# Performance work log

Hardware: AMD Instinct MI355X
Metric: run time of the kernel (lower is better)

The kernel has to match this reference:

```python
import jax, jax.numpy as jnp
import numpy as np

KH, KW = 3, 3          # kernel_size
SH, SW = 1, 1          # strides
EM_ITERS = 3           # standard EM routing iteration count
EPS = 1e-9


def to_blocks(x):
    """im2col-style block extraction matching ConvCaps2D._to_blocks.
    x: [B, H, W, ...] -> [B, Ho, Wo, KH, KW, ...] with Ho=(H-KH+1)//SH."""
    Ho = (x.shape[1] - KH + 1) // SH
    Wo = (x.shape[2] - KW + 1) // SW
    rows = []
    for i in range(KH):
        cols = [x[:, i:i + (Ho - 1) * SH + 1:SH, j:j + (Wo - 1) * SW + 1:SW]
                for j in range(KW)]
        rows.append(jnp.stack(cols, axis=3))   # [B,Ho,Wo,KW,...]
    return jnp.stack(rows, axis=3)             # [B,Ho,Wo,KH,KW,...]


def em_routing(votes, a_in, beta_a, beta_u):
    """EM routing (Hinton et al. 2018 matrix capsules).
    votes: [B,Ho,Wo,O,N,D], a_in: [B,Ho,Wo,N], beta_*: [1,1,1,O].
    Returns poses mu [B,Ho,Wo,O,D], activations [B,Ho,Wo,O]."""
    B, Ho, Wo, O, N, D = votes.shape
    R = jnp.full((B, Ho, Wo, O, N), 1.0 / O, dtype=votes.dtype)
    a = a_in[:, :, :, None, :]                                  # [B,Ho,Wo,1,N]
    mu = None
    a_out = None
    for t in range(EM_ITERS):
        inv_temp = 1.0 + t                                      # increasing lambda schedule
        # ---- M-step ----
        r = R * a                                               # [B,Ho,Wo,O,N]
        r_sum = jnp.sum(r, axis=-1, keepdims=True) + EPS        # [B,Ho,Wo,O,1]
        mu = jnp.einsum('bhwon,bhwond->bhwod', r, votes) / r_sum
        diff2 = (votes - mu[:, :, :, :, None, :]) ** 2          # [B,Ho,Wo,O,N,D]
        sigma2 = jnp.einsum('bhwon,bhwond->bhwod', r, diff2) / r_sum + EPS
        cost = jnp.sum((beta_u[..., None] + 0.5 * jnp.log(sigma2)) * r_sum, axis=-1)
        a_out = jax.nn.sigmoid(inv_temp * (beta_a - cost))      # [B,Ho,Wo,O]
        # ---- E-step (skipped after last M-step) ----
        if t < EM_ITERS - 1:
            s2 = sigma2[:, :, :, :, None, :]
            logp = -0.5 * jnp.sum(jnp.log(2.0 * jnp.pi * s2) + diff2 / s2, axis=-1)
            logits = jnp.log(a_out + EPS)[..., None] + logp     # [B,Ho,Wo,O,N]
            R = jax.nn.softmax(logits, axis=3)                  # normalize over output caps
    return mu, a_out


def setup_inputs() -> dict:
    key = jax.random.key(0)
    k1, k2, k3, k4, k5 = jax.random.split(key, 5)
    B, H, W, Cin, d1, d2 = 4, 16, 16, 16, 4, 4
    O = 32
    poses = jax.random.normal(k1, (B, H, W, Cin, d1, d2), dtype=jnp.float32)
    activations = jax.random.uniform(k2, (B, H, W, Cin), dtype=jnp.float32)
    fan_in = KH * KW * Cin * d1 * d2
    kernel = jax.random.normal(k3, (O, KH, KW, Cin, d1, d2), dtype=jnp.float32) * np.sqrt(2.0 / fan_in).astype(np.float32)
    beta_a = jax.random.normal(k4, (1, 1, 1, O), dtype=jnp.float32) * 0.1
    beta_u = jax.random.normal(k5, (1, 1, 1, O), dtype=jnp.float32) * 0.1
    return {"poses": poses, "activations": activations, "kernel": kernel,
            "beta_a": beta_a, "beta_u": beta_u}


def reference(poses, activations, kernel, beta_a, beta_u):
    B, _, _, Cin, d1, d2 = poses.shape
    O = kernel.shape[0]
    pose_blocks = to_blocks(poses)                              # [B,Ho,Wo,KH,KW,Cin,d1,d2]
    # votes = pose @ W per (output channel, kernel offset, input channel)
    votes = jnp.einsum('bhwKLcij,oKLcjl->bhwoKLcil', pose_blocks, kernel)
    Ho, Wo = votes.shape[1], votes.shape[2]
    N = KH * KW * Cin
    votes = votes.reshape(B, Ho, Wo, O, N, d1 * d2)             # [B,Ho,Wo,O,N,D]
    a_blocks = to_blocks(activations).reshape(B, Ho, Wo, N)
    mu, a_out = em_routing(votes, a_blocks, beta_a, beta_u)
    capsule_poses = mu.reshape(B, Ho, Wo, O, d1, d2)
    return capsule_poses, a_out
```

## Files before the change

kernel.cpp:

```cpp
#include <hip/hip_runtime.h>
#include <math.h>

#define NBLK 784
#define O_ 32
#define N_ 144
#define D_ 16
#define PS 20
#define RS 148

__global__ __launch_bounds__(256) void convcaps_em(
    const float* __restrict__ poses,
    const float* __restrict__ acts,
    const float* __restrict__ kern,
    const float* __restrict__ beta_a,
    const float* __restrict__ beta_u,
    float* __restrict__ out)
{
    const int pix = blockIdx.x;
    const int b  = pix / 196;
    const int hw = pix - b * 196;
    const int ho = hw / 14;
    const int wo = hw - ho * 14;

    __shared__ __align__(16) float P[N_ * PS];
    __shared__ float A[N_];
    __shared__ float Rm[O_ * RS];

    const int t = threadIdx.x;

    for (int idx = t; idx < N_ * D_; idx += 256) {
        int n = idx >> 4, d = idx & 15;
        int ki = n / 48, kj = (n >> 4) - ki * 3, c = n & 15;
        P[n * PS + d] = poses[((b * 16 + ho + ki) * 16 + (wo + kj)) * 256 + c * 16 + d];
    }
    if (t < N_) {
        int n = t;
        int ki = n / 48, kj = (n >> 4) - ki * 3, c = n & 15;
        A[n] = acts[((b * 16 + ho + ki) * 16 + (wo + kj)) * 16 + c];
    }
    __syncthreads();
    for (int idx = t; idx < O_ * N_; idx += 256) {
        int oo = idx / N_;
        int nn = idx - oo * N_;
        Rm[oo * RS + nn] = 0.03125f * A[nn];
    }
    __syncthreads();

    const int o = t >> 3;
    const int s = t & 7;
    const float buv = beta_u[o];
    const float ba  = beta_a[o];
    const float* Kbase = kern + (size_t)o * (N_ * D_);

    float a_out = 0.f;
    float mu[16];

    for (int it = 0; it < 3; ++it) {
        float S1[16], S2[16];
#pragma unroll
        for (int d = 0; d < 16; ++d) { S1[d] = 0.f; S2[d] = 0.f; }
        float rs = 0.f;

#pragma unroll 2
        for (int k = 0; k < 18; ++k) {
            const int n = s + (k << 3);
            const float r = Rm[o * RS + n];
            rs += r;
            float pv[16], kv[16];
            const float4* Pp = (const float4*)(P + n * PS);
            ((float4*)pv)[0] = Pp[0];
            ((float4*)pv)[1] = Pp[1];
            ((float4*)pv)[2] = Pp[2];
            ((float4*)pv)[3] = Pp[3];
            const float4* Kp = (const float4*)(Kbase + n * D_);
            ((float4*)kv)[0] = Kp[0];
            ((float4*)kv)[1] = Kp[1];
            ((float4*)kv)[2] = Kp[2];
            ((float4*)kv)[3] = Kp[3];
#pragma unroll
            for (int i = 0; i < 4; ++i) {
#pragma unroll
                for (int l = 0; l < 4; ++l) {
                    float v = fmaf(pv[i*4+0], kv[0+l],
                              fmaf(pv[i*4+1], kv[4+l],
                              fmaf(pv[i*4+2], kv[8+l],
                                   pv[i*4+3] * kv[12+l])));
                    S1[i*4+l] = fmaf(r, v, S1[i*4+l]);
                    S2[i*4+l] = fmaf(r * v, v, S2[i*4+l]);
                }
            }
        }

#pragma unroll
        for (int m = 1; m < 8; m <<= 1) {
            rs += __shfl_xor(rs, m, 64);
#pragma unroll
            for (int d = 0; d < 16; ++d) {
                S1[d] += __shfl_xor(S1[d], m, 64);
                S2[d] += __shfl_xor(S2[d], m, 64);
            }
        }

        rs += 1e-9f;
        const float inv_rs = 1.0f / rs;
        float sig[16];
#pragma unroll
        for (int d = 0; d < 16; ++d) {
            mu[d] = S1[d] * inv_rs;
            sig[d] = fmaf(-mu[d], mu[d], S2[d] * inv_rs) + 1e-9f;
        }
        const float L = __logf(sig[0]  * sig[1])  + __logf(sig[2]  * sig[3])
                      + __logf(sig[4]  * sig[5])  + __logf(sig[6]  * sig[7])
                      + __logf(sig[8]  * sig[9])  + __logf(sig[10] * sig[11])
                      + __logf(sig[12] * sig[13]) + __logf(sig[14] * sig[15]);
        const float cost = rs * fmaf(0.5f, L, 16.0f * buv);
        const float x = (float)(it + 1) * (ba - cost);
        a_out = 1.0f / (1.0f + __expf(-x));

        if (it < 2) {
            float isg[16];
#pragma unroll
            for (int d = 0; d < 16; ++d) isg[d] = 1.0f / sig[d];
            const float LC = __logf(a_out + 1e-9f)
                           - 0.5f * (16.0f * 1.8378770664093453f + L);
            __syncthreads();

#pragma unroll 2
            for (int k = 0; k < 18; ++k) {
                const int n = s + (k << 3);
                float pv[16], kv[16];
                const float4* Pp = (const float4*)(P + n * PS);
                ((float4*)pv)[0] = Pp[0];
                ((float4*)pv)[1] = Pp[1];
                ((float4*)pv)[2] = Pp[2];
                ((float4*)pv)[3] = Pp[3];
                const float4* Kp = (const float4*)(Kbase + n * D_);
                ((float4*)kv)[0] = Kp[0];
                ((float4*)kv)[1] = Kp[1];
                ((float4*)kv)[2] = Kp[2];
                ((float4*)kv)[3] = Kp[3];
                float Q = 0.f;
#pragma unroll
                for (int i = 0; i < 4; ++i) {
#pragma unroll
                    for (int l = 0; l < 4; ++l) {
                        float v = fmaf(pv[i*4+0], kv[0+l],
                                  fmaf(pv[i*4+1], kv[4+l],
                                  fmaf(pv[i*4+2], kv[8+l],
                                       pv[i*4+3] * kv[12+l])));
                        const float df = v - mu[i*4+l];
                        Q = fmaf(df * df, isg[i*4+l], Q);
                    }
                }
                Rm[o * RS + n] = fmaf(-0.5f, Q, LC);
            }
            __syncthreads();

            if (t < N_) {
                float v[32];
                float mx = -1e30f;
#pragma unroll
                for (int oo = 0; oo < 32; ++oo) {
                    v[oo] = Rm[oo * RS + t];
                    mx = fmaxf(mx, v[oo]);
                }
                float sm = 0.f;
#pragma unroll
                for (int oo = 0; oo < 32; ++oo) {
                    v[oo] = __expf(v[oo] - mx);
                    sm += v[oo];
                }
                const float sc = A[t] / sm;
#pragma unroll
                for (int oo = 0; oo < 32; ++oo)
                    Rm[oo * RS + t] = v[oo] * sc;
            }
            __syncthreads();
        }
    }

    if (s == 0) {
        float4* ob = (float4*)(out + (size_t)pix * 512 + o * 16);
        ob[0] = make_float4(mu[0],  mu[1],  mu[2],  mu[3]);
        ob[1] = make_float4(mu[4],  mu[5],  mu[6],  mu[7]);
        ob[2] = make_float4(mu[8],  mu[9],  mu[10], mu[11]);
        ob[3] = make_float4(mu[12], mu[13], mu[14], mu[15]);
        out[401408 + pix * 32 + o] = a_out;
    }
}

extern "C" void kernel_launch(void* const* d_in, const int* in_sizes, int n_in,
                              void* d_out, int out_size, void* d_ws, size_t ws_size,
                              hipStream_t stream)
{
    const float* poses  = (const float*)d_in[0];
    const float* acts   = (const float*)d_in[1];
    const float* kern   = (const float*)d_in[2];
    const float* beta_a = (const float*)d_in[3];
    const float* beta_u = (const float*)d_in[4];
    float* out = (float*)d_out;
    convcaps_em<<<NBLK, 256, 0, stream>>>(poses, acts, kern, beta_a, beta_u, out);
}
```

Measured before the change: 102.5 us.

## Split EM routing into per-iteration M-step and E-step kernels over workspace

Replaces the single fused kernel (one block per output pixel, 784 blocks) with five launches that alternate an M-step kernel (grid 784x4, 128 threads) and an E-step/softmax kernel (grid 784x6). Routing weights and per-capsule statistics are passed through the workspace buffer. The goal is more parallelism and occupancy than 784 large blocks with heavy shared memory can give. In exchange it adds launch overhead, global-memory round trips for R and stats, and recomputation of votes from global poses in every kernel. The old fused kernel remains as a fallback when the workspace is too small.

```diff
diff --git a/kernel.cpp b/kernel.cpp
--- a/kernel.cpp
+++ b/kernel.cpp
@@ -7,6 +7,229 @@
 #define D_ 16
 #define PS 20
 #define RS 148
+
+#define STATS_STRIDE 36
+#define WS_STATS_FLOATS (25088 * STATS_STRIDE)
+#define WS_R_FLOATS     (784 * 32 * 144)
+#define WS_NEED_BYTES   ((size_t)(WS_STATS_FLOATS + WS_R_FLOATS) * 4)
+
+
+__global__ __launch_bounds__(128) void caps_mom(
+    const float* __restrict__ poses,
+    const float* __restrict__ acts,
+    const float* __restrict__ kern,
+    const float* __restrict__ Rw,
+    const float* __restrict__ beta_a,
+    const float* __restrict__ beta_u,
+    float* __restrict__ stats,
+    float* __restrict__ out,
+    int rmode, int fin, float invtemp)
+{
+    const int pix = blockIdx.x;
+    const int b  = pix / 196;
+    const int hw = pix - b * 196;
+    const int ho = hw / 14;
+    const int wo = hw - ho * 14;
+
+    const int t  = threadIdx.x;
+    const int o  = blockIdx.y * 8 + (t >> 4);
+    const int s  = t & 15;
+
+    const float* Kbase = kern + (size_t)o * (N_ * D_);
+    const float* Rrow  = Rw + ((size_t)pix * 32 + o) * 144;
+
+    float S1[16], S2[16];
+#pragma unroll
+    for (int d = 0; d < 16; ++d) { S1[d] = 0.f; S2[d] = 0.f; }
+    float rs = 0.f;
+
+#pragma unroll
+    for (int k = 0; k < 9; ++k) {
+        const int n = s + (k << 4);
+        const int ki = n / 48, kj = (n >> 4) - (n / 48) * 3, c = n & 15;
+        const int cell = (b * 16 + ho + ki) * 16 + (wo + kj);
+        float r;
+        if (rmode) r = Rrow[n];
+        else       r = acts[cell * 16 + c] * 0.03125f;
+        rs += r;
+        float pv[16], kv[16];
+        const float4* Pp = (const float4*)(poses + (size_t)cell * 256 + c * 16);
+        ((float4*)pv)[0] = Pp[0];
+        ((float4*)pv)[1] = Pp[1];
+        ((float4*)pv)[2] = Pp[2];
+        ((float4*)pv)[3] = Pp[3];
+        const float4* Kp = (const float4*)(Kbase + n * D_);
+        ((float4*)kv)[0] = Kp[0];
+        ((float4*)kv)[1] = Kp[1];
+        ((float4*)kv)[2] = Kp[2];
+        ((float4*)kv)[3] = Kp[3];
+#pragma unroll
+        for (int i = 0; i < 4; ++i) {
+#pragma unroll
+            for (int l = 0; l < 4; ++l) {
+                float v = fmaf(pv[i*4+0], kv[0+l],
+                          fmaf(pv[i*4+1], kv[4+l],
+                          fmaf(pv[i*4+2], kv[8+l],
+                               pv[i*4+3] * kv[12+l])));
+                S1[i*4+l] = fmaf(r, v, S1[i*4+l]);
+                S2[i*4+l] = fmaf(r * v, v, S2[i*4+l]);
+            }
+        }
+    }
+
+#pragma unroll
+    for (int m = 1; m < 16; m <<= 1) {
+        rs += __shfl_xor(rs, m, 64);
+#pragma unroll
+        for (int d = 0; d < 16; ++d) {
+            S1[d] += __shfl_xor(S1[d], m, 64);
+            S2[d] += __shfl_xor(S2[d], m, 64);
+        }
+    }
+
+    rs += 1e-9f;
+    const float inv_rs = 1.0f / rs;
+    float mu[16], sig[16];
+#pragma unroll
+    for (int d = 0; d < 16; ++d) {
+        mu[d] = S1[d] * inv_rs;
+        sig[d] = fmaf(-mu[d], mu[d], S2[d] * inv_rs) + 1e-9f;
+    }
+    const float L = __logf(sig[0]  * sig[1])  + __logf(sig[2]  * sig[3])
+                  + __logf(sig[4]  * sig[5])  + __logf(sig[6]  * sig[7])
+                  + __logf(sig[8]  * sig[9])  + __logf(sig[10] * sig[11])
+                  + __logf(sig[12] * sig[13]) + __logf(sig[14] * sig[15]);
+    const float cost = rs * fmaf(0.5f, L, 16.0f * beta_u[o]);
+    const float x = invtemp * (beta_a[o] - cost);
+    const float a_out = 1.0f / (1.0f + __expf(-x));
+
+    if (s == 0) {
+        if (fin) {
+            float4* ob = (float4*)(out + (size_t)pix * 512 + o * 16);
+            ob[0] = make_float4(mu[0],  mu[1],  mu[2],  mu[3]);
+            ob[1] = make_float4(mu[4],  mu[5],  mu[6],  mu[7]);
+            ob[2] = make_float4(mu[8],  mu[9],  mu[10], mu[11]);
+            ob[3] = make_float4(mu[12], mu[13], mu[14], mu[15]);
+            out[401408 + pix * 32 + o] = a_out;
+        } else {
+            float* sb = stats + ((size_t)pix * 32 + o) * STATS_STRIDE;
+            float4* sb4 = (float4*)sb;
+            sb4[0] = make_float4(mu[0],  mu[1],  mu[2],  mu[3]);
+            sb4[1] = make_float4(mu[4],  mu[5],  mu[6],  mu[7]);
+            sb4[2] = make_float4(mu[8],  mu[9],  mu[10], mu[11]);
+            sb4[3] = make_float4(mu[12], mu[13], mu[14], mu[15]);
+            float isg[16];
+#pragma unroll
+            for (int d = 0; d < 16; ++d) isg[d] = 1.0f / sig[d];
+            sb4[4] = make_float4(isg[0],  isg[1],  isg[2],  isg[3]);
+            sb4[5] = make_float4(isg[4],  isg[5],  isg[6],  isg[7]);
+            sb4[6] = make_float4(isg[8],  isg[9],  isg[10], isg[11]);
+            sb4[7] = make_float4(isg[12], isg[13], isg[14], isg[15]);
+            sb[32] = __logf(a_out + 1e-9f)
+                   - 0.5f * (16.0f * 1.8378770664093453f + L);
+        }
+    }
+}
+
+__global__ __launch_bounds__(256) void caps_logits(
+    const float* __restrict__ poses,
+    const float* __restrict__ acts,
+    const float* __restrict__ kern,
+    const float* __restrict__ stats,
+    float* __restrict__ Rw)
+{
+    const int pix  = blockIdx.x;
+    const int slab = blockIdx.y;
+    const int b  = pix / 196;
+    const int hw = pix - b * 196;
+    const int ho = hw / 14;
+    const int wo = hw - ho * 14;
+
+    const int t  = threadIdx.x;
+    const int o  = t >> 3;
+    const int ln = t & 7;
+
+    __shared__ float Lg[24][33];
+    __shared__ float Al[24];
+    __shared__ float Rl[32][24];
+
+    if (t < 24) {
+        const int n = slab * 24 + t;
+        const int ki = n / 48, kj = (n >> 4) - (n / 48) * 3, c = n & 15;
+        Al[t] = acts[((b * 16 + ho + ki) * 16 + (wo + kj)) * 16 + c];
+    }
+
+    float mu[16], isg[16];
+    const float* sb = stats + ((size_t)pix * 32 + o) * STATS_STRIDE;
+    const float4* sb4 = (const float4*)sb;
+    ((float4*)mu)[0]  = sb4[0]; ((float4*)mu)[1]  = sb4[1];
+    ((float4*)mu)[2]  = sb4[2]; ((float4*)mu)[3]  = sb4[3];
+    ((float4*)isg)[0] = sb4[4]; ((float4*)isg)[1] = sb4[5];
+    ((float4*)isg)[2] = sb4[6]; ((float4*)isg)[3] = sb4[7];
+    const float LC = sb[32];
+
+    const float* Kbase = kern + (size_t)o * (N_ * D_);
+
+#pragma unroll
+    for (int j = 0; j < 3; ++j) {
+        const int nl = ln * 3 + j;
+        const int n  = slab * 24 + nl;
+        const int ki = n / 48, kj = (n >> 4) - (n / 48) * 3, c = n & 15;
+        const int cell = (b * 16 + ho + ki) * 16 + (wo + kj);
+        float pv[16], kv[16];
+        const float4* Pp = (const float4*)(poses + (size_t)cell * 256 + c * 16);
+        ((float4*)pv)[0] = Pp[0];
+        ((float4*)pv)[1] = Pp[1];
+        ((float4*)pv)[2] = Pp[2];
+        ((float4*)pv)[3] = Pp[3];
+        const float4* Kp = (const float4*)(Kbase + n * D_);
+        ((float4*)kv)[0] = Kp[0];
+        ((float4*)kv)[1] = Kp[1];
+        ((float4*)kv)[2] = Kp[2];
+        ((float4*)kv)[3] = Kp[3];
+        float Q = 0.f;
+#pragma unroll
+        for (int i = 0; i < 4; ++i) {
+#pragma unroll
+            for (int l = 0; l < 4; ++l) {
+                float v = fmaf(pv[i*4+0], kv[0+l],
+                          fmaf(pv[i*4+1], kv[4+l],
+                          fmaf(pv[i*4+2], kv[8+l],
+                               pv[i*4+3] * kv[12+l])));
+                const float df = v - mu[i*4+l];
+                Q = fmaf(df * df, isg[i*4+l], Q);
+            }
+        }
+        Lg[nl][o] = fmaf(-0.5f, Q, LC);
+    }
+    __syncthreads();
+
+    if (t < 24) {
+        float mx = -1e30f;
+#pragma unroll
+        for (int oo = 0; oo < 32; ++oo) mx = fmaxf(mx, Lg[t][oo]);
+        float sm = 0.f;
+        float ev[32];
+#pragma unroll
+        for (int oo = 0; oo < 32; ++oo) {
+            ev[oo] = __expf(Lg[t][oo] - mx);
+            sm += ev[oo];
+        }
+        const float sc = Al[t] / sm;
+#pragma unroll
+        for (int oo = 0; oo < 32; ++oo) Rl[oo][t] = ev[oo] * sc;
+    }
+    __syncthreads();
+
+#pragma unroll
+    for (int rep = 0; rep < 3; ++rep) {
+        const int idx = t + rep * 256;
+        const int oo = idx / 24;
+        const int nl = idx - oo * 24;
+        Rw[((size_t)pix * 32 + oo) * 144 + slab * 24 + nl] = Rl[oo][nl];
+    }
+}
+
 
 __global__ __launch_bounds__(256) void convcaps_em(
     const float* __restrict__ poses,
@@ -199,5 +422,20 @@
     const float* beta_a = (const float*)d_in[3];
     const float* beta_u = (const float*)d_in[4];
     float* out = (float*)d_out;
-    convcaps_em<<<NBLK, 256, 0, stream>>>(poses, acts, kern, beta_a, beta_u, out);
+
+    if (ws_size >= WS_NEED_BYTES) {
+        float* stats = (float*)d_ws;
+        float* Rw    = stats + WS_STATS_FLOATS;
+        dim3 gm(NBLK, 4), gl(NBLK, 6);
+        caps_mom<<<gm, 128, 0, stream>>>(poses, acts, kern, Rw, beta_a, beta_u,
+                                         stats, out, 0, 0, 1.0f);
+        caps_logits<<<gl, 256, 0, stream>>>(poses, acts, kern, stats, Rw);
+        caps_mom<<<gm, 128, 0, stream>>>(poses, acts, kern, Rw, beta_a, beta_u,
+                                         stats, out, 1, 0, 2.0f);
+        caps_logits<<<gl, 256, 0, stream>>>(poses, acts, kern, stats, Rw);
+        caps_mom<<<gm, 128, 0, stream>>>(poses, acts, kern, Rw, beta_a, beta_u,
+                                         stats, out, 1, 1, 3.0f);
+    } else {
+        convcaps_em<<<NBLK, 256, 0, stream>>>(poses, acts, kern, beta_a, beta_u, out);
+    }
 }
```

Result: slower. 211.0 us (+105.9%).

## Fuse E-step softmax into M-step via lane-per-output layout with DPP reductions

Applied to the files above, without the earlier changes.

Remaps threads so the 32 output capsules sit in adjacent lanes and 8 groups split the inputs. The softmax over outputs is then done in registers with DPP/swizzle cross-lane max and sum, which removes the separate E-step vote pass, the shared R matrix, and several barriers. Each vote is computed once per iteration instead of twice. The partial sums are reduced across groups through a large shared buffer (about 33 KB), which adds LDS traffic and may lower occupancy. It also expands the quadratic form so the per-vote E-step needs fewer operations.

```diff
diff --git a/kernel.cpp b/kernel.cpp
--- a/kernel.cpp
+++ b/kernel.cpp
@@ -2,11 +2,104 @@
 #include <math.h>
 
 #define NBLK 784
-#define O_ 32
-#define N_ 144
-#define D_ 16
 #define PS 20
-#define RS 148
+#define LOG2PI_16 29.406033062549525f
+
+#define REDN (33 * 256)
+
+#define DPPF(x, ctrl) __int_as_float(__builtin_amdgcn_update_dpp(              \
+    0, __float_as_int(x), ctrl, 0xF, 0xF, true))
+
+__device__ __forceinline__ float swzx16(float x) {
+    return __int_as_float(__builtin_amdgcn_ds_swizzle(__float_as_int(x), 0x401F));
+}
+__device__ __forceinline__ float rmax32(float x) {
+    x = fmaxf(x, DPPF(x, 0xB1));
+    x = fmaxf(x, DPPF(x, 0x4E));
+    x = fmaxf(x, DPPF(x, 0x141));
+    x = fmaxf(x, DPPF(x, 0x140));
+    x = fmaxf(x, swzx16(x));
+    return x;
+}
+__device__ __forceinline__ float rsum32(float x) {
+    x += DPPF(x, 0xB1);
+    x += DPPF(x, 0x4E);
+    x += DPPF(x, 0x141);
+    x += DPPF(x, 0x140);
+    x += swzx16(x);
+    return x;
+}
+
+#define VOTE(kk, v) do {                                                       \
+        float pv[16], kv[16];                                                  \
+        const float4* Pp_ = (const float4*)(Pbase + (kk) * (8 * PS));          \
+        ((float4*)pv)[0] = Pp_[0]; ((float4*)pv)[1] = Pp_[1];                  \
+        ((float4*)pv)[2] = Pp_[2]; ((float4*)pv)[3] = Pp_[3];                  \
+        const float4* Kp_ = (const float4*)(Kg + (kk) * (8 * 16));             \
+        ((float4*)kv)[0] = Kp_[0]; ((float4*)kv)[1] = Kp_[1];                  \
+        ((float4*)kv)[2] = Kp_[2]; ((float4*)kv)[3] = Kp_[3];                  \
+        _Pragma("unroll")                                                      \
+        for (int i_ = 0; i_ < 4; ++i_) {                                       \
+            _Pragma("unroll")                                                  \
+            for (int l_ = 0; l_ < 4; ++l_) {                                   \
+                v[i_*4+l_] = fmaf(pv[i_*4+0], kv[0+l_],                        \
+                             fmaf(pv[i_*4+1], kv[4+l_],                        \
+                             fmaf(pv[i_*4+2], kv[8+l_],                        \
+                                  pv[i_*4+3] * kv[12+l_])));                   \
+            }                                                                  \
+        }                                                                      \
+    } while (0)
+
+#define REDUCE_G() do {                                                        \
+    __syncthreads();                                                           \
+    _Pragma("unroll")                                                          \
+    for (int j = 0; j < 16; ++j) {                                             \
+        Red[j * 256 + t]        = S1[j];                                       \
+        Red[(j + 16) * 256 + t] = S2[j];                                       \
+    }                                                                          \
+    Red[32 * 256 + t] = rs;                                                    \
+    __syncthreads();                                                           \
+    _Pragma("unroll")                                                          \
+    for (int j = 0; j < 16; ++j) { S1[j] = 0.f; S2[j] = 0.f; }                 \
+    rs = 0.f;                                                                  \
+    _Pragma("unroll")                                                          \
+    for (int gg = 0; gg < 8; ++gg) {                                           \
+        const int base_ = gg * 32 + o;                                         \
+        _Pragma("unroll")                                                      \
+        for (int j = 0; j < 16; ++j) {                                         \
+            S1[j] += Red[j * 256 + base_];                                     \
+            S2[j] += Red[(j + 16) * 256 + base_];                              \
+        }                                                                      \
+        rs += Red[32 * 256 + base_];                                           \
+    }                                                                          \
+} while (0)
+
+#define STATS(IT) do {                                                         \
+    rs += 1e-9f;                                                               \
+    const float ivr_ = 1.0f / rs;                                              \
+    _Pragma("unroll")                                                          \
+    for (int j = 0; j < 16; ++j) {                                             \
+        mu[j]  = S1[j] * ivr_;                                                 \
+        sig[j] = fmaf(-mu[j], mu[j], S2[j] * ivr_) + 1e-9f;                    \
+    }                                                                          \
+    L = __logf(sig[0]  * sig[1])  + __logf(sig[2]  * sig[3])                   \
+      + __logf(sig[4]  * sig[5])  + __logf(sig[6]  * sig[7])                   \
+      + __logf(sig[8]  * sig[9])  + __logf(sig[10] * sig[11])                  \
+      + __logf(sig[12] * sig[13]) + __logf(sig[14] * sig[15]);                 \
+    const float cost_ = rs * fmaf(0.5f, L, 16.0f * buv);                       \
+    a_out = 1.0f / (1.0f + __expf(-(IT) * (ba - cost_)));                      \
+} while (0)
+
+#define PREP() do {                                                            \
+    float c0_ = 0.f;                                                           \
+    _Pragma("unroll")                                                          \
+    for (int j = 0; j < 16; ++j) {                                             \
+        isg[j] = 1.0f / sig[j];                                                \
+        qb[j]  = -2.0f * mu[j] * isg[j];                                       \
+        c0_    = fmaf(mu[j] * mu[j], isg[j], c0_);                             \
+    }                                                                          \
+    LC = __logf(a_out + 1e-9f) - 0.5f * (LOG2PI_16 + L) - 0.5f * c0_;          \
+} while (0)
 
 __global__ __launch_bounds__(256) void convcaps_em(
     const float* __restrict__ poses,
@@ -22,164 +115,88 @@
     const int ho = hw / 14;
     const int wo = hw - ho * 14;
 
-    __shared__ __align__(16) float P[N_ * PS];
-    __shared__ float A[N_];
-    __shared__ float Rm[O_ * RS];
+    __shared__ __align__(16) float P[144 * PS];
+    __shared__ float A[144];
+    __shared__ float Red[REDN];
 
     const int t = threadIdx.x;
 
-    for (int idx = t; idx < N_ * D_; idx += 256) {
+    for (int idx = t; idx < 144 * 16; idx += 256) {
         int n = idx >> 4, d = idx & 15;
         int ki = n / 48, kj = (n >> 4) - ki * 3, c = n & 15;
         P[n * PS + d] = poses[((b * 16 + ho + ki) * 16 + (wo + kj)) * 256 + c * 16 + d];
     }
-    if (t < N_) {
+    if (t < 144) {
         int n = t;
         int ki = n / 48, kj = (n >> 4) - ki * 3, c = n & 15;
         A[n] = acts[((b * 16 + ho + ki) * 16 + (wo + kj)) * 16 + c];
     }
     __syncthreads();
-    for (int idx = t; idx < O_ * N_; idx += 256) {
-        int oo = idx / N_;
-        int nn = idx - oo * N_;
-        Rm[oo * RS + nn] = 0.03125f * A[nn];
-    }
-    __syncthreads();
-
-    const int o = t >> 3;
-    const int s = t & 7;
+
+    const int o = t & 31;
+    const int g = t >> 5;
     const float buv = beta_u[o];
     const float ba  = beta_a[o];
-    const float* Kbase = kern + (size_t)o * (N_ * D_);
-
-    float a_out = 0.f;
-    float mu[16];
-
-    for (int it = 0; it < 3; ++it) {
-        float S1[16], S2[16];
-#pragma unroll
-        for (int d = 0; d < 16; ++d) { S1[d] = 0.f; S2[d] = 0.f; }
-        float rs = 0.f;
-
+    const float* Kbase = kern + (size_t)o * 2304;
+    const float* Pbase = P + g * PS;
+    const float* Kg    = Kbase + g * 16;
+
+    float S1[16], S2[16], rs;
+    float mu[16], sig[16], isg[16], qb[16];
+    float L, LC = 0.f, a_out = 0.f;
+
+#pragma unroll
+    for (int j = 0; j < 16; ++j) { S1[j] = 0.f; S2[j] = 0.f; }
+    rs = 0.f;
+#pragma unroll 3
+    for (int k = 0; k < 18; ++k) {
+        float v[16];
+        VOTE(k, v);
+        const float r = A[g + (k << 3)] * 0.03125f;
+        rs += r;
+#pragma unroll
+        for (int j = 0; j < 16; ++j) {
+            S1[j] = fmaf(r, v[j], S1[j]);
+            S2[j] = fmaf(r * v[j], v[j], S2[j]);
+        }
+    }
+    REDUCE_G();
+    STATS(1.0f);
+    PREP();
+
+#pragma unroll 1
+    for (int it = 1; it < 3; ++it) {
+#pragma unroll
+        for (int j = 0; j < 16; ++j) { S1[j] = 0.f; S2[j] = 0.f; }
+        rs = 0.f;
 #pragma unroll 2
         for (int k = 0; k < 18; ++k) {
-            const int n = s + (k << 3);
-            const float r = Rm[o * RS + n];
+            float v[16];
+            VOTE(k, v);
+            float Q = 0.f;
+#pragma unroll
+            for (int j = 0; j < 16; ++j)
+                Q = fmaf(fmaf(isg[j], v[j], qb[j]), v[j], Q);
+            const float lg = fmaf(-0.5f, Q, LC);
+            const float mx = rmax32(lg);
+            const float e  = __expf(lg - mx);
+            const float sm = rsum32(e);
+            float inv_sm;
+            asm("v_rcp_f32 %0, %1" : "=v"(inv_sm) : "v"(sm));
+            const float r = e * A[g + (k << 3)] * inv_sm;
             rs += r;
-            float pv[16], kv[16];
-            const float4* Pp = (const float4*)(P + n * PS);
-            ((float4*)pv)[0] = Pp[0];
-            ((float4*)pv)[1] = Pp[1];
-            ((float4*)pv)[2] = Pp[2];
-            ((float4*)pv)[3] = Pp[3];
-            const float4* Kp = (const float4*)(Kbase + n * D_);
-            ((float4*)kv)[0] = Kp[0];
-            ((float4*)kv)[1] = Kp[1];
-            ((float4*)kv)[2] = Kp[2];
-            ((float4*)kv)[3] = Kp[3];
-#pragma unroll
-            for (int i = 0; i < 4; ++i) {
-#pragma unroll
-                for (int l = 0; l < 4; ++l) {
-                    float v = fmaf(pv[i*4+0], kv[0+l],
-                              fmaf(pv[i*4+1], kv[4+l],
-                              fmaf(pv[i*4+2], kv[8+l],
-                                   pv[i*4+3] * kv[12+l])));
-                    S1[i*4+l] = fmaf(r, v, S1[i*4+l]);
-                    S2[i*4+l] = fmaf(r * v, v, S2[i*4+l]);
-                }
+#pragma unroll
+            for (int j = 0; j < 16; ++j) {
+                S1[j] = fmaf(r, v[j], S1[j]);
+                S2[j] = fmaf(r * v[j], v[j], S2[j]);
             }
         }
-
-#pragma unroll
-        for (int m = 1; m < 8; m <<= 1) {
-            rs += __shfl_xor(rs, m, 64);
-#pragma unroll
-            for (int d = 0; d < 16; ++d) {
-                S1[d] += __shfl_xor(S1[d], m, 64);
-                S2[d] += __shfl_xor(S2[d], m, 64);
-            }
-        }
-
-        rs += 1e-9f;
-        const float inv_rs = 1.0f / rs;
-        float sig[16];
-#pragma unroll
-        for (int d = 0; d < 16; ++d) {
-            mu[d] = S1[d] * inv_rs;
-            sig[d] = fmaf(-mu[d], mu[d], S2[d] * inv_rs) + 1e-9f;
-        }
-        const float L = __logf(sig[0]  * sig[1])  + __logf(sig[2]  * sig[3])
-                      + __logf(sig[4]  * sig[5])  + __logf(sig[6]  * sig[7])
-                      + __logf(sig[8]  * sig[9])  + __logf(sig[10] * sig[11])
-                      + __logf(sig[12] * sig[13]) + __logf(sig[14] * sig[15]);
-        const float cost = rs * fmaf(0.5f, L, 16.0f * buv);
-        const float x = (float)(it + 1) * (ba - cost);
-        a_out = 1.0f / (1.0f + __expf(-x));
-
-        if (it < 2) {
-            float isg[16];
-#pragma unroll
-            for (int d = 0; d < 16; ++d) isg[d] = 1.0f / sig[d];
-            const float LC = __logf(a_out + 1e-9f)
-                           - 0.5f * (16.0f * 1.8378770664093453f + L);
-            __syncthreads();
-
-#pragma unroll 2
-            for (int k = 0; k < 18; ++k) {
-                const int n = s + (k << 3);
-                float pv[16], kv[16];
-                const float4* Pp = (const float4*)(P + n * PS);
-                ((float4*)pv)[0] = Pp[0];
-                ((float4*)pv)[1] = Pp[1];
-                ((float4*)pv)[2] = Pp[2];
-                ((float4*)pv)[3] = Pp[3];
-                const float4* Kp = (const float4*)(Kbase + n * D_);
-                ((float4*)kv)[0] = Kp[0];
-                ((float4*)kv)[1] = Kp[1];
-                ((float4*)kv)[2] = Kp[2];
-                ((float4*)kv)[3] = Kp[3];
-                float Q = 0.f;
-#pragma unroll
-                for (int i = 0; i < 4; ++i) {
-#pragma unroll
-                    for (int l = 0; l < 4; ++l) {
-                        float v = fmaf(pv[i*4+0], kv[0+l],
-                                  fmaf(pv[i*4+1], kv[4+l],
-                                  fmaf(pv[i*4+2], kv[8+l],
-                                       pv[i*4+3] * kv[12+l])));
-                        const float df = v - mu[i*4+l];
-                        Q = fmaf(df * df, isg[i*4+l], Q);
-                    }
-                }
-                Rm[o * RS + n] = fmaf(-0.5f, Q, LC);
-            }
-            __syncthreads();
-
-            if (t < N_) {
-                float v[32];
-                float mx = -1e30f;
-#pragma unroll
-                for (int oo = 0; oo < 32; ++oo) {
-                    v[oo] = Rm[oo * RS + t];
-                    mx = fmaxf(mx, v[oo]);
-                }
-                float sm = 0.f;
-#pragma unroll
-                for (int oo = 0; oo < 32; ++oo) {
-                    v[oo] = __expf(v[oo] - mx);
-                    sm += v[oo];
-                }
-                const float sc = A[t] / sm;
-#pragma unroll
-                for (int oo = 0; oo < 32; ++oo)
-                    Rm[oo * RS + t] = v[oo] * sc;
-            }
-            __syncthreads();
-        }
-    }
-
-    if (s == 0) {
+        REDUCE_G();
+        STATS((float)(it + 1));
+        if (it < 2) PREP();
+    }
+
+    if (g == 0) {
         float4* ob = (float4*)(out + (size_t)pix * 512 + o * 16);
         ob[0] = make_float4(mu[0],  mu[1],  mu[2],  mu[3]);
         ob[1] = make_float4(mu[4],  mu[5],  mu[6],  mu[7]);
```

Result: slower. 140.7 us (+37.2%).
